# Kernel tuning notes

Measured on AMD Instinct MI355X. Metric: run time of the kernel, lower is better.

Reference implementation:

```python
import jax, jax.numpy as jnp
import numpy as np
from jax import lax

B, C, L = 2048, 9605, 8
WL_PER_LABEL = 50
ALPHA = 0.5        # training_config['alpha4']
ALPHA1 = 0.1       # margin
ALPHA2 = 2.0       # training_config['alpha2']
ALPHA3 = 10.0      # training_config['alpha3']
ALPHA_OTHER = 0.5
NEG = jnp.float32(-1e30)


def setup_inputs() -> dict:
    key = jax.random.key(0)
    k1, k2, k3, k4 = jax.random.split(key, 4)
    x = jax.random.normal(k1, (B, C), dtype=jnp.float32) * 2.0
    y = (jax.random.uniform(k2, (B, C)) < 0.005).astype(jnp.float32)
    y_neg = (jax.random.uniform(k3, (B, C)) < 0.005).astype(jnp.float32)
    # whitelist masks: L app-labels, each whitelisting ~WL_PER_LABEL raw classes
    idx = jax.random.randint(k4, (L, WL_PER_LABEL), 0, C)
    wl_masks = jnp.zeros((L, C), dtype=bool).at[jnp.arange(L)[:, None], idx].set(True)
    return {"x": x, "y": y, "y_neg": y_neg, "wl_masks": wl_masks}


def reference(x, y, y_neg, wl_masks):
    # y_neg is consumed by the original forward (find_gt_whitelist) but never
    # affects the returned loss, faithfully ignored here.
    xs_pos = jax.nn.sigmoid(x)                                  # [B, C]
    # top_k_thres = max(11th-largest sigmoid, alpha_other)
    thres = jnp.maximum(lax.top_k(xs_pos, 11)[0][:, 10], ALPHA_OTHER)  # [B]
    # per-label whitelist max: m[b,l] = max_{c in wl_l} xs_pos[b,c]
    m = jnp.max(jnp.where(wl_masks[None, :, :], xs_pos[:, None, :], NEG), axis=-1)  # [B, L]
    # label l is a ground-truth whitelist label iff y has any positive in wl_l
    has_pos = jnp.einsum('bc,lc->bl', y, wl_masks.astype(y.dtype)) > 0   # [B, L]
    correct_max = jnp.max(jnp.where(has_pos, m, NEG), axis=-1)           # [B]
    incorrect_max = jnp.max(jnp.where(~has_pos, m, NEG), axis=-1)        # [B]
    any_correct = jnp.any(has_pos, axis=-1)
    any_incorrect = jnp.any(~has_pos, axis=-1)
    # union whitelist max (the "other" branch uses xs_pos over all wl indices)
    union_max = jnp.max(jnp.where(jnp.any(wl_masks, axis=0)[None, :], xs_pos, NEG), axis=-1)
    x1 = jnp.where(any_correct, correct_max, thres)
    x2 = jnp.where(any_correct,
                   jnp.where(any_incorrect, jnp.maximum(incorrect_max, thres), thres),
                   union_max)
    coef = jnp.where(any_correct, 1.0, 1.0 - ALPHA)
    d = x2 - x1 + ALPHA1
    rank = jnp.where(d > 0, ALPHA2, 1.0) * jax.nn.sigmoid(ALPHA3 * d)
    return jnp.mean(coef * rank)
```

## Files before the change

### kernel.cpp

```cpp
#include <hip/hip_runtime.h>

#define CC 9605
#define BB 2048
#define LL 8
#define NEGF (-1e30f)
#define NINF (-__builtin_huge_valf())

#define WS_PARTIALS_OFF 16384

__device__ __forceinline__ unsigned enc_f(float f) {
  unsigned u = __float_as_uint(f);
  return (u & 0x80000000u) ? ~u : (u | 0x80000000u);
}
__device__ __forceinline__ float dec_u(unsigned e) {
  unsigned u = (e & 0x80000000u) ? (e & 0x7fffffffu) : ~e;
  return __uint_as_float(u);
}
__device__ __forceinline__ float sigm(float z) {
  return 1.0f / (1.0f + __expf(-z));
}

__global__ void wl_sniff(const unsigned* __restrict__ wlw,
                         unsigned* __restrict__ wsu) {
  const int nwords = (LL * CC) / 4;
  const int stride = gridDim.x * blockDim.x;
  unsigned f = 0u;
  for (int j = blockIdx.x * blockDim.x + threadIdx.x; j < nwords; j += stride) {
    unsigned w = wlw[j];
#pragma unroll
    for (int k = 0; k < 4; ++k) {
      unsigned b = (w >> (8 * k)) & 255u;
      if (b == 1u)    { f |= 2u; if (k != 0) f |= 1u; }
      if (b == 0x3fu) { f |= 8u; if (k == 1) f |= 4u; }
    }
  }
#pragma unroll
  for (int off = 32; off >= 1; off >>= 1) f |= __shfl_xor(f, off, 64);
  if ((threadIdx.x & 63) == 0 && f) atomicOr(&wsu[1], f);
}

__global__ void wl_compact(const unsigned char* __restrict__ wl,
                           unsigned* __restrict__ wsu) {
  const int tid = threadIdx.x;
  const int lane = tid & 63;
  const int c = blockIdx.x * 256 + tid;
  const unsigned g = wsu[1];
  const int dt = (g & 1u) ? 0 : (g & 4u) ? 3 : (g & 2u) ? 1 : (g & 8u) ? 2 : 0;
  const int* wl32 = (const int*)wl;
  const float* wlf = (const float*)wl;
  const unsigned short* wlh = (const unsigned short*)wl;
  unsigned m = 0u;
  if (c < CC) {
#pragma unroll
    for (int l = 0; l < LL; ++l) {
      int j = l * CC + c;
      bool on;
      if (dt == 0) on = (wl[j] != 0);
      else if (dt == 1) on = (wl32[j] != 0);
      else if (dt == 2) on = (wlf[j] != 0.0f);
      else on = (wlh[j] != 0);
      if (on) m |= (1u << l);
    }
  }
  unsigned long long bal = __ballot(m != 0u);
  if (bal) {
    unsigned wcnt = (unsigned)__popcll(bal);
    unsigned basep = 0u;
    if (lane == 0) basep = atomicAdd(&wsu[0], wcnt);
    basep = __shfl(basep, 0, 64);
    if (m) {
      unsigned pos = basep + (unsigned)__popcll(bal & ((1ull << lane) - 1ull));
      if (pos < 2048u) wsu[4 + pos] = ((unsigned)c << 8) | m;
    }
  }
}


#define FOR11(OP) OP(0) OP(1) OP(2) OP(3) OP(4) OP(5) OP(6) OP(7) OP(8) OP(9) OP(10)
#define FOR8(OP) OP(0) OP(1) OP(2) OP(3) OP(4) OP(5) OP(6) OP(7)

#define DECL_S(k) float s_##k = NINF;
#define INS1(k) { float _hi = fmaxf(s_##k, cv); cv = fminf(s_##k, cv); s_##k = _hi; }
#define TOP11V(v) { float cv = (v); FOR11(INS1) }
#define TOP4(T) { TOP11V((T).x) TOP11V((T).y) TOP11V((T).z) TOP11V((T).w) }

__global__ __launch_bounds__(256) void loss_kernel(
    const float* __restrict__ x, const float* __restrict__ y,
    const unsigned* __restrict__ wsu, float* __restrict__ partials) {
  const int tid = threadIdx.x;
  const int lane = tid & 63;
  const int wid = tid >> 6;
  const int r = blockIdx.x * 4 + wid;
  const long long base = (long long)r * CC;

  const unsigned nu = min(wsu[0], 2048u);
  const unsigned* ents = wsu + 4;
  unsigned entv[7];
  float gxv[7], gyv[7];
#pragma unroll
  for (int k = 0; k < 7; ++k) {
    unsigned e = (unsigned)lane + 64u * (unsigned)k;
    entv[k] = (e < nu) ? ents[e] : 0u;
  }
#pragma unroll
  for (int k = 0; k < 7; ++k) {
    int col = (int)(entv[k] >> 8);
    gxv[k] = x[base + col];
    gyv[k] = y[base + col];
  }

  const int soff = (4 - (r & 3)) & 3;
  const int ng = (CC - soff) >> 2;
  const int rem = ng - 2368;
  const int tailn = CC - soff - (ng << 2);
  const int m_extra = soff + tailn;
  const float4* vp = (const float4*)(x + base + soff);

  FOR11(DECL_S)

  float4 a0 = vp[lane];
  float4 a1 = vp[lane + 64];
  float4 a2 = vp[lane + 128];
  float4 a3 = vp[lane + 192];
  int gb = lane;
  for (int i = 0; i + 8 <= 37; i += 4) {
    float4 b0 = vp[gb + 256];
    float4 b1 = vp[gb + 320];
    float4 b2 = vp[gb + 384];
    float4 b3 = vp[gb + 448];
    TOP4(a0) TOP4(a1) TOP4(a2) TOP4(a3)
    a0 = b0; a1 = b1; a2 = b2; a3 = b3;
    gb += 256;
  }
  TOP4(a0) TOP4(a1) TOP4(a2) TOP4(a3)
  {
    float4 t = vp[lane + 2304];
    TOP4(t)
  }
  {
    float4 t = make_float4(NINF, NINF, NINF, NINF);
    if (lane < rem) t = vp[2368 + lane];
    TOP4(t)
  }
  {
    float tv = NINF;
    if (lane < m_extra) {
      int tc = (lane < soff) ? lane : (soff + (ng << 2) + (lane - soff));
      tv = x[base + tc];
    }
    TOP11V(tv)
  }

#define DECL_E(k) unsigned e_##k = enc_f(s_##k);
  FOR11(DECL_E)
  unsigned wlo = e_10;
  unsigned whi = e_0;
#pragma unroll
  for (int off = 32; off >= 1; off >>= 1) {
    wlo = max(wlo, __shfl_xor(wlo, off, 64));
    whi = max(whi, __shfl_xor(whi, off, 64));
  }
  unsigned lo = wlo, hi = whi + 1u;
  while (hi - lo > 1u) {
    unsigned mid = lo + ((hi - lo) >> 1);
    unsigned cnt = 0u;
#define CMP1(k) cnt += (e_##k >= mid) ? 1u : 0u;
    FOR11(CMP1)
#undef CMP1
    unsigned tot = (unsigned)__popcll(__ballot(cnt & 1u)) +
                   ((unsigned)__popcll(__ballot(cnt & 2u)) << 1) +
                   ((unsigned)__popcll(__ballot(cnt & 4u)) << 2) +
                   ((unsigned)__popcll(__ballot(cnt & 8u)) << 3);
    if (tot >= 11u) lo = mid; else hi = mid;
  }
  const unsigned E11 = lo;

#define DECL_LM(k) float lm_##k = NEGF;
  FOR8(DECL_LM)
  unsigned pmask = 0u;
#pragma unroll
  for (int k = 0; k < 7; ++k) {
    unsigned mk = entv[k] & 255u;
    pmask |= mk;
    if (gyv[k] > 0.0f) pmask |= (mk << 8);
#define FOLD1(l) if ((mk >> l) & 1u) lm_##l = fmaxf(lm_##l, gxv[k]);
    FOR8(FOLD1)
#undef FOLD1
  }
  for (unsigned e = (unsigned)lane + 448u; e < nu; e += 64u) {
    unsigned ent = ents[e];
    unsigned mk = ent & 255u;
    float xv = x[base + (ent >> 8)];
    float yv = y[base + (ent >> 8)];
    pmask |= mk;
    if (yv > 0.0f) pmask |= (mk << 8);
#define FOLD1(l) if ((mk >> l) & 1u) lm_##l = fmaxf(lm_##l, xv);
    FOR8(FOLD1)
#undef FOLD1
  }
#pragma unroll
  for (int off = 32; off >= 1; off >>= 1) {
    pmask |= __shfl_xor(pmask, off, 64);
#define RED1(l) lm_##l = fmaxf(lm_##l, __shfl_xor(lm_##l, off, 64));
    FOR8(RED1)
#undef RED1
  }

  if (lane == 0) {
    unsigned PR = pmask & 255u, PO = (pmask >> 8) & 255u;
    float thres = fmaxf(sigm(dec_u(E11)), 0.5f);
    float cmax = NEGF, imax = NEGF, umax = NEGF;
#define EP1(l)                                                   \
    if ((PR >> l) & 1u) {                                        \
      float ml = sigm(lm_##l);                                   \
      umax = fmaxf(umax, ml);                                    \
      if ((PO >> l) & 1u) cmax = fmaxf(cmax, ml);                \
      else imax = fmaxf(imax, ml);                               \
    }
    FOR8(EP1)
#undef EP1
    bool anyc = (PO != 0u);
    bool anyi = (PO != 255u);
    float x1 = anyc ? cmax : thres;
    float x2 = anyc ? (anyi ? fmaxf(imax, thres) : thres)
                    : ((nu > 0u) ? umax : NEGF);
    float coef = anyc ? 1.0f : 0.5f;
    float dd = x2 - x1 + 0.1f;
    float rank = ((dd > 0.0f) ? 2.0f : 1.0f) * sigm(10.0f * dd);
    partials[r] = coef * rank;
  }
}

__global__ void final_reduce(const float* __restrict__ partials,
                             float* __restrict__ out) {
  __shared__ float sh[4];
  const int tid = threadIdx.x;
  const int lane = tid & 63;
  const int wid = tid >> 6;
  float s = 0.0f;
  for (int i = tid; i < BB; i += 256) s += partials[i];
#pragma unroll
  for (int off = 32; off >= 1; off >>= 1) s += __shfl_xor(s, off, 64);
  if (lane == 0) sh[wid] = s;
  __syncthreads();
  if (tid == 0) out[0] = (sh[0] + sh[1] + sh[2] + sh[3]) * (1.0f / (float)BB);
}

extern "C" void kernel_launch(void* const* d_in, const int* in_sizes, int n_in,
                              void* d_out, int out_size, void* d_ws,
                              size_t ws_size, hipStream_t stream) {
  const float* x = (const float*)d_in[0];
  const float* y = (const float*)d_in[1];
  const unsigned char* wl = (const unsigned char*)d_in[3];
  float* out = (float*)d_out;
  unsigned* wsu = (unsigned*)d_ws;
  float* partials = (float*)((char*)d_ws + WS_PARTIALS_OFF);

  hipMemsetAsync(d_ws, 0, 16, stream);
  wl_sniff<<<64, 256, 0, stream>>>((const unsigned*)wl, wsu);
  wl_compact<<<(CC + 255) / 256, 256, 0, stream>>>(wl, wsu);
  loss_kernel<<<BB / 4, 256, 0, stream>>>(x, y, wsu, partials);
  final_reduce<<<1, 256, 0, stream>>>(partials, out);
}
```

Measured before the change: 234.0 us.

## Split each row across two wavefronts and merge top-11 via shared memory

Each row is now processed by a 128-thread block of two wavefronts instead of one wavefront per row. Each wave scans half the row's float4 groups for its per-lane top-11 and half of the whitelist gather entries. The second wave writes its per-lane top lists and label maxima to LDS, and the first wave merges them before the binary-search threshold and epilogue. This doubles the wave count to shorten per-wave serial latency, at the cost of a __syncthreads, an LDS merge pass, and __launch_bounds__(128,1), which may limit occupancy.

```diff
diff --git a/kernel.cpp b/kernel.cpp
--- a/kernel.cpp
+++ b/kernel.cpp
@@ -77,37 +77,29 @@
 
 
 #define FOR11(OP) OP(0) OP(1) OP(2) OP(3) OP(4) OP(5) OP(6) OP(7) OP(8) OP(9) OP(10)
+#define FOR11I(OP) OP(0) OP(1) OP(2) OP(3) OP(4) OP(5) OP(6) OP(7) OP(8) OP(9) OP(10)
 #define FOR8(OP) OP(0) OP(1) OP(2) OP(3) OP(4) OP(5) OP(6) OP(7)
 
 #define DECL_S(k) float s_##k = NINF;
 #define INS1(k) { float _hi = fmaxf(s_##k, cv); cv = fminf(s_##k, cv); s_##k = _hi; }
-#define TOP11V(v) { float cv = (v); FOR11(INS1) }
+#define TOP11V(v) { float cv = (v); FOR11I(INS1) }
 #define TOP4(T) { TOP11V((T).x) TOP11V((T).y) TOP11V((T).z) TOP11V((T).w) }
 
-__global__ __launch_bounds__(256) void loss_kernel(
+__global__ __launch_bounds__(128, 1) void loss_kernel(
     const float* __restrict__ x, const float* __restrict__ y,
     const unsigned* __restrict__ wsu, float* __restrict__ partials) {
+  __shared__ float sh_top[64][11];
+  __shared__ float sh_w1lm[8];
+  __shared__ unsigned sh_w1pm;
+
   const int tid = threadIdx.x;
   const int lane = tid & 63;
-  const int wid = tid >> 6;
-  const int r = blockIdx.x * 4 + wid;
+  const int w = tid >> 6;
+  const int r = blockIdx.x;
   const long long base = (long long)r * CC;
 
   const unsigned nu = min(wsu[0], 2048u);
   const unsigned* ents = wsu + 4;
-  unsigned entv[7];
-  float gxv[7], gyv[7];
-#pragma unroll
-  for (int k = 0; k < 7; ++k) {
-    unsigned e = (unsigned)lane + 64u * (unsigned)k;
-    entv[k] = (e < nu) ? ents[e] : 0u;
-  }
-#pragma unroll
-  for (int k = 0; k < 7; ++k) {
-    int col = (int)(entv[k] >> 8);
-    gxv[k] = x[base + col];
-    gyv[k] = y[base + col];
-  }
 
   const int soff = (4 - (r & 3)) & 3;
   const int ng = (CC - soff) >> 2;
@@ -118,12 +110,14 @@
 
   FOR11(DECL_S)
 
-  float4 a0 = vp[lane];
-  float4 a1 = vp[lane + 64];
-  float4 a2 = vp[lane + 128];
-  float4 a3 = vp[lane + 192];
-  int gb = lane;
-  for (int i = 0; i + 8 <= 37; i += 4) {
+  const int g0 = w ? 1216 : 0;
+  float4 a0 = vp[g0 + lane];
+  float4 a1 = vp[g0 + lane + 64];
+  float4 a2 = vp[g0 + lane + 128];
+  float4 a3 = vp[g0 + lane + 192];
+  int gb = g0 + lane;
+#pragma unroll 1
+  for (int it = 0; it < 3; ++it) {
     float4 b0 = vp[gb + 256];
     float4 b1 = vp[gb + 320];
     float4 b2 = vp[gb + 384];
@@ -132,27 +126,96 @@
     a0 = b0; a1 = b1; a2 = b2; a3 = b3;
     gb += 256;
   }
-  TOP4(a0) TOP4(a1) TOP4(a2) TOP4(a3)
-  {
-    float4 t = vp[lane + 2304];
-    TOP4(t)
-  }
-  {
-    float4 t = make_float4(NINF, NINF, NINF, NINF);
-    if (lane < rem) t = vp[2368 + lane];
-    TOP4(t)
-  }
-  {
+  if (w == 0) {
+    float4 b0 = vp[gb + 256];
+    float4 b1 = vp[gb + 320];
+    float4 b2 = vp[gb + 384];
+    TOP4(a0) TOP4(a1) TOP4(a2) TOP4(a3)
+    TOP4(b0) TOP4(b1) TOP4(b2)
+  } else {
+    float4 b0 = vp[gb + 256];
+    float4 b1 = vp[gb + 320];
+    float4 tr = make_float4(NINF, NINF, NINF, NINF);
+    if (lane < rem) tr = vp[2368 + lane];
     float tv = NINF;
     if (lane < m_extra) {
       int tc = (lane < soff) ? lane : (soff + (ng << 2) + (lane - soff));
       tv = x[base + tc];
     }
+    TOP4(a0) TOP4(a1) TOP4(a2) TOP4(a3)
+    TOP4(b0) TOP4(b1) TOP4(tr)
     TOP11V(tv)
   }
+
+  unsigned en0, en1, en2, en3;
+  {
+    unsigned e0 = (unsigned)lane + 64u * (unsigned)w;
+    en0 = (e0 < nu) ? ents[e0] : 0u;
+    en1 = (e0 + 128u < nu) ? ents[e0 + 128u] : 0u;
+    en2 = (e0 + 256u < nu) ? ents[e0 + 256u] : 0u;
+    en3 = (e0 + 384u < nu) ? ents[e0 + 384u] : 0u;
+  }
+  float gx0 = x[base + (en0 >> 8)], gy0 = y[base + (en0 >> 8)];
+  float gx1 = x[base + (en1 >> 8)], gy1 = y[base + (en1 >> 8)];
+  float gx2 = x[base + (en2 >> 8)], gy2 = y[base + (en2 >> 8)];
+  float gx3 = x[base + (en3 >> 8)], gy3 = y[base + (en3 >> 8)];
+
+#define DECL_LM(k) float lm_##k = NEGF;
+  FOR8(DECL_LM)
+  unsigned pmask = 0u;
+#define FOLDE(EN, GX, GY)                                        \
+  {                                                              \
+    unsigned mk = (EN) & 255u;    \
+    pmask |= mk;                                                 \
+    if ((GY) > 0.0f) pmask |= (mk << 8);                         \
+    if (mk & 1u)   lm_0 = fmaxf(lm_0, (GX));                     \
+    if (mk & 2u)   lm_1 = fmaxf(lm_1, (GX));                     \
+    if (mk & 4u)   lm_2 = fmaxf(lm_2, (GX));                     \
+    if (mk & 8u)   lm_3 = fmaxf(lm_3, (GX));                     \
+    if (mk & 16u)  lm_4 = fmaxf(lm_4, (GX));                     \
+    if (mk & 32u)  lm_5 = fmaxf(lm_5, (GX));                     \
+    if (mk & 64u)  lm_6 = fmaxf(lm_6, (GX));                     \
+    if (mk & 128u) lm_7 = fmaxf(lm_7, (GX));                     \
+  }
+  FOLDE(en0, gx0, gy0)
+  FOLDE(en1, gx1, gy1)
+  FOLDE(en2, gx2, gy2)
+  FOLDE(en3, gx3, gy3)
+  for (unsigned e = 512u + (unsigned)tid; e < nu; e += 128u) {
+    unsigned ent = ents[e];
+    float xv = x[base + (ent >> 8)];
+    float yv = y[base + (ent >> 8)];
+    FOLDE(ent, xv, yv)
+  }
+#pragma unroll
+  for (int off = 32; off >= 1; off >>= 1) {
+    pmask |= __shfl_xor(pmask, off, 64);
+#define RED1(l) lm_##l = fmaxf(lm_##l, __shfl_xor(lm_##l, off, 64));
+    FOR8(RED1)
+#undef RED1
+  }
+
+  if (w == 1) {
+#define ST1(k) sh_top[lane][k] = s_##k;
+    FOR11(ST1)
+#undef ST1
+    if (lane == 0) {
+#define STL(l) sh_w1lm[l] = lm_##l;
+      FOR8(STL)
+#undef STL
+      sh_w1pm = pmask;
+    }
+  }
+  __syncthreads();
+  if (w != 0) return;
+
+#define MG1(k) TOP11V(sh_top[lane][k])
+  FOR11(MG1)
+#undef MG1
 
 #define DECL_E(k) unsigned e_##k = enc_f(s_##k);
   FOR11(DECL_E)
+#undef DECL_E
   unsigned wlo = e_10;
   unsigned whi = e_0;
 #pragma unroll
@@ -175,38 +238,11 @@
   }
   const unsigned E11 = lo;
 
-#define DECL_LM(k) float lm_##k = NEGF;
-  FOR8(DECL_LM)
-  unsigned pmask = 0u;
-#pragma unroll
-  for (int k = 0; k < 7; ++k) {
-    unsigned mk = entv[k] & 255u;
-    pmask |= mk;
-    if (gyv[k] > 0.0f) pmask |= (mk << 8);
-#define FOLD1(l) if ((mk >> l) & 1u) lm_##l = fmaxf(lm_##l, gxv[k]);
-    FOR8(FOLD1)
-#undef FOLD1
-  }
-  for (unsigned e = (unsigned)lane + 448u; e < nu; e += 64u) {
-    unsigned ent = ents[e];
-    unsigned mk = ent & 255u;
-    float xv = x[base + (ent >> 8)];
-    float yv = y[base + (ent >> 8)];
-    pmask |= mk;
-    if (yv > 0.0f) pmask |= (mk << 8);
-#define FOLD1(l) if ((mk >> l) & 1u) lm_##l = fmaxf(lm_##l, xv);
-    FOR8(FOLD1)
-#undef FOLD1
-  }
-#pragma unroll
-  for (int off = 32; off >= 1; off >>= 1) {
-    pmask |= __shfl_xor(pmask, off, 64);
-#define RED1(l) lm_##l = fmaxf(lm_##l, __shfl_xor(lm_##l, off, 64));
-    FOR8(RED1)
-#undef RED1
-  }
-
   if (lane == 0) {
+    pmask |= sh_w1pm;
+#define CMB(l) lm_##l = fmaxf(lm_##l, sh_w1lm[l]);
+    FOR8(CMB)
+#undef CMB
     unsigned PR = pmask & 255u, PO = (pmask >> 8) & 255u;
     float thres = fmaxf(sigm(dec_u(E11)), 0.5f);
     float cmax = NEGF, imax = NEGF, umax = NEGF;
@@ -259,6 +295,6 @@
   hipMemsetAsync(d_ws, 0, 16, stream);
   wl_sniff<<<64, 256, 0, stream>>>((const unsigned*)wl, wsu);
   wl_compact<<<(CC + 255) / 256, 256, 0, stream>>>(wl, wsu);
-  loss_kernel<<<BB / 4, 256, 0, stream>>>(x, y, wsu, partials);
+  loss_kernel<<<BB, 128, 0, stream>>>(x, y, wsu, partials);
   final_reduce<<<1, 256, 0, stream>>>(partials, out);
 }
```

Result: faster. 222.9 us (-4.8%).
